# Kernel optimization log

Measured on AMD Instinct MI355X. Metric: run time of the kernel, lower is better.

Reference implementation:

```python
import jax, jax.numpy as jnp
import numpy as np

EPS_XVAR = 1e-06
EPS_QVAR = 1e-05
EPS_VAR = 1e-05
MIN_SCALE = 0.1  # rbf kernel
EPS_EDGE = 1e-06


def setup_inputs() -> dict:
    key = jax.random.key(0)
    k1, k2, k3, k4 = jax.random.split(key, 4)
    B, O, I, M = 2048, 64, 64, 32
    x = jax.random.normal(k1, (B, I), dtype=jnp.float32)
    # inducing locations: linspace(-1.5, 1.5, M) tiled over (O, I)
    z = jnp.broadcast_to(jnp.linspace(-1.5, 1.5, M, dtype=jnp.float32), (O, I, M))
    q_mu = jax.random.normal(k2, (O, I, M), dtype=jnp.float32) * 0.05
    q_log_var = jnp.full((O, I, M), -3.0, dtype=jnp.float32)
    log_scale = jnp.zeros((O, I), dtype=jnp.float32)
    log_variance = jnp.full((O, I), -1.0, dtype=jnp.float32)
    return {"x": x, "z": z, "q_mu": q_mu, "q_log_var": q_log_var,
            "log_scale": log_scale, "log_variance": log_variance}


def reference(x, z, q_mu, q_log_var, log_scale, log_variance):
    # x: [B, I]; params: [O, I, M] or [O, I]
    x_mean = x
    x_var = jnp.zeros_like(x) + EPS_XVAR

    q_var = jnp.maximum(jnp.exp(q_log_var), EPS_QVAR)           # [O, I, M]
    var_kern = jnp.maximum(jnp.exp(log_variance), EPS_VAR)      # [O, I]
    lengthscale = jnp.maximum(jnp.exp(log_scale), MIN_SCALE)    # [O, I]

    x_mu_exp = x_mean[:, None, :, None]        # [B, 1, I, 1]
    x_var_exp = x_var[:, None, :, None]        # [B, 1, I, 1]
    ell_sq = (lengthscale ** 2)[None, :, :, None]  # [1, O, I, 1]
    vk = var_kern[None, :, :, None]            # [1, O, I, 1]

    denom = ell_sq + x_var_exp                 # [B, O, I, 1]
    diff = x_mu_exp - z[None]                  # [B, O, I, M]
    psi_1 = vk * jnp.sqrt(ell_sq / denom) * jnp.exp(-0.5 * diff ** 2 / denom)

    edge_means = jnp.sum(psi_1 * q_mu[None], axis=-1)                      # [B, O, I]
    edge_vars = jnp.sum(psi_1 ** 2 * (q_var + q_mu ** 2)[None], axis=-1)   # [B, O, I]
    edge_vars = jnp.maximum(edge_vars - edge_means ** 2, EPS_EDGE)

    return edge_means.sum(axis=2), edge_vars.sum(axis=2)  # each [B, O]
```

## Files before the change

### kernel.cpp

```cpp
#include <hip/hip_runtime.h>

#define BATCH 2048
#define ODIM 64
#define IDIM 64
#define MDIM 32

static constexpr float LOG2E = 1.4426950408889634f;

#if __has_builtin(__builtin_amdgcn_exp2f)
#define EXP2F(x) __builtin_amdgcn_exp2f(x)
#else
#define EXP2F(x) exp2f(x)
#endif

typedef float v2f __attribute__((ext_vector_type(2)));

__global__ __launch_bounds__(256) void prep_kernel(
    const float* __restrict__ x, const float* __restrict__ z,
    const float* __restrict__ q_mu, const float* __restrict__ q_log_var,
    const float* __restrict__ log_scale, const float* __restrict__ log_variance,
    float2* __restrict__ cm, float4* __restrict__ aux, float* __restrict__ xT)
{
    const int bx = blockIdx.x;
    if (bx < 512) {
        int tid = bx * 256 + threadIdx.x;
        int oi  = tid >> 5;
        int m   = tid & (MDIM - 1);

        float ls   = log_scale[oi];
        float lv   = log_variance[oi];
        float ell  = fmaxf(expf(ls), 0.1f);
        float ell2 = ell * ell;
        float vk   = fmaxf(expf(lv), 1e-5f);
        float denom = ell2 + 1e-6f;
        float A    = vk * sqrtf(ell2 / denom);
        float a    = -0.5f * LOG2E / denom;

        float qm = q_mu[tid];
        float qv = fmaxf(expf(q_log_var[tid]), 1e-5f);

        float zm = z[tid];
        float w  = exp2f(a * zm * zm);

        float2 c;
        c.x = A * qm * w;
        c.y = A * A * (qv + qm * qm) * w * w;
        cm[tid] = c;

        if (m == 0) {
            float z0 = z[oi * MDIM + 0];
            float z1 = z[oi * MDIM + 1];
            float dz = z1 - z0;
            float4 Ax = {a, -2.0f * a * z0, -2.0f * a * dz, 0.0f};
            aux[oi] = Ax;
        }
    } else {
        int tid = (bx - 512) * 256 + threadIdx.x;
        int i = tid >> 11;
        int b = tid & (BATCH - 1);
        xT[tid] = x[b * IDIM + i];
    }
}

__global__ __launch_bounds__(512, 8) void gpkan_main_kernel(
    const float* __restrict__ xT, const float2* __restrict__ cm,
    const float4* __restrict__ aux, float* __restrict__ out)
{
    const int o     = blockIdx.x & (ODIM - 1);
    const int btile = blockIdx.x >> 6;
    const int lane  = threadIdx.x & 63;
    const int wave  = __builtin_amdgcn_readfirstlane(threadIdx.x >> 6);
    const int b0    = btile * 128 + lane;
    const int i0    = wave * 8;

    __shared__ float2 lcm[8][256];
    __shared__ float4 laux[8][8];
    __shared__ float  smr[8][2][64];
    __shared__ float  svr[8][2][64];

    const float2* __restrict__ Cg = cm + ((size_t)o * IDIM + i0) * MDIM;
    #pragma unroll
    for (int r = 0; r < 4; ++r)
        lcm[wave][lane + 64 * r] = Cg[lane + 64 * r];
    if (lane < 8) laux[wave][lane] = aux[o * IDIM + i0 + lane];

    v2f emt = {0.f, 0.f};
    v2f evt = {0.f, 0.f};

    v2f xv;
    xv.x = xT[i0 * BATCH + b0];
    xv.y = xT[i0 * BATCH + b0 + 64];

    #pragma unroll 1
    for (int ii = 0; ii < 8; ++ii) {
        int inext = i0 + ((ii + 1) & 7);
        v2f xn;
        xn.x = xT[inext * BATCH + b0];
        xn.y = xT[inext * BATCH + b0 + 64];

        const float4 Ax = laux[wave][ii];
        v2f e1 = {Ax.x, Ax.x}, e2 = {Ax.y, Ax.y}, rc = {Ax.z, Ax.z};

        v2f t = __builtin_elementwise_fma(e1, xv, e2) * xv;
        v2f Eb;
        Eb.x = EXP2F(t.x); Eb.y = EXP2F(t.y);
        v2f ur = rc * xv;
        v2f rr;
        rr.x = EXP2F(ur.x); rr.y = EXP2F(ur.y);

        v2f s = rr * rr;
        v2f u = s * s;

        v2f Pe = {0.f, 0.f}, Po = {0.f, 0.f};
        v2f Qe = {0.f, 0.f}, Qo = {0.f, 0.f};

        const float4* C = (const float4*)&lcm[wave][ii * MDIM];
        #pragma unroll
        for (int k = 15; k >= 0; --k) {
            float4 c = C[k];
            v2f c1e = {c.x, c.x}, c2e = {c.y, c.y};
            v2f c1o = {c.z, c.z}, c2o = {c.w, c.w};
            Pe = __builtin_elementwise_fma(Pe, s, c1e);
            Po = __builtin_elementwise_fma(Po, s, c1o);
            Qe = __builtin_elementwise_fma(Qe, u, c2e);
            Qo = __builtin_elementwise_fma(Qo, u, c2o);
        }

        v2f P = __builtin_elementwise_fma(rr, Po, Pe);
        v2f Q = __builtin_elementwise_fma(s,  Qo, Qe);

        v2f em_i = Eb * P;
        v2f Eb2  = Eb * Eb;
        v2f ev_i = Eb2 * Q;

        v2f eps = {1e-6f, 1e-6f};
        v2f d   = __builtin_elementwise_fma(-em_i, em_i, ev_i);
        evt += __builtin_elementwise_max(d, eps);
        emt += em_i;

        xv = xn;
    }

    smr[wave][0][lane] = emt.x;
    smr[wave][1][lane] = emt.y;
    svr[wave][0][lane] = evt.x;
    svr[wave][1][lane] = evt.y;
    __syncthreads();

    if (threadIdx.x < 128) {
        const int half = threadIdx.x >> 6;
        const int l    = threadIdx.x & 63;
        float em = 0.f, ev = 0.f;
        #pragma unroll
        for (int w = 0; w < 8; ++w) {
            em += smr[w][half][l];
            ev += svr[w][half][l];
        }
        const int bb = btile * 128 + half * 64 + l;
        out[bb * ODIM + o]                = em;
        out[BATCH * ODIM + bb * ODIM + o] = ev;
    }
}

extern "C" void kernel_launch(void* const* d_in, const int* in_sizes, int n_in,
                              void* d_out, int out_size, void* d_ws, size_t ws_size,
                              hipStream_t stream) {
    const float* x            = (const float*)d_in[0];
    const float* z            = (const float*)d_in[1];
    const float* q_mu         = (const float*)d_in[2];
    const float* q_log_var    = (const float*)d_in[3];
    const float* log_scale    = (const float*)d_in[4];
    const float* log_variance = (const float*)d_in[5];
    float* out = (float*)d_out;

    char* ws = (char*)d_ws;
    float2* cm  = (float2*)ws;
    float4* aux = (float4*)(ws + (size_t)ODIM * IDIM * MDIM * sizeof(float2));
    float*  xT  = (float*)(ws + (size_t)ODIM * IDIM * MDIM * sizeof(float2)
                              + (size_t)ODIM * IDIM * sizeof(float4));

    prep_kernel<<<dim3(1024), dim3(256), 0, stream>>>(
        x, z, q_mu, q_log_var, log_scale, log_variance, cm, aux, xT);
    gpkan_main_kernel<<<dim3((BATCH / 128) * ODIM), dim3(512), 0, stream>>>(
        xT, cm, aux, out);
}
```

Baseline: 83.65 us.

## Fuse parameter prep and x transpose into main kernel via shared memory

Removes the separate prep kernel and its global workspace. Each block now transposes its 128-row x tile into shared memory and computes the per-(o,i,m) coefficients and per-(o,i) aux constants directly into LDS before the main loop. This saves a kernel launch and the global round trip for cm, aux and xT. In exchange every one of the 16 batch tiles recomputes the coefficient exps for its output column, and the larger LDS footprint lowers the launch-bound occupancy target from 8 to 6.

```diff
diff --git a/kernel.cpp b/kernel.cpp
--- a/kernel.cpp
+++ b/kernel.cpp
@@ -15,17 +15,44 @@
 
 typedef float v2f __attribute__((ext_vector_type(2)));
 
-__global__ __launch_bounds__(256) void prep_kernel(
+__global__ __launch_bounds__(512, 6) void gpkan_fused_kernel(
     const float* __restrict__ x, const float* __restrict__ z,
     const float* __restrict__ q_mu, const float* __restrict__ q_log_var,
     const float* __restrict__ log_scale, const float* __restrict__ log_variance,
-    float2* __restrict__ cm, float4* __restrict__ aux, float* __restrict__ xT)
+    float* __restrict__ out)
 {
-    const int bx = blockIdx.x;
-    if (bx < 512) {
-        int tid = bx * 256 + threadIdx.x;
-        int oi  = tid >> 5;
-        int m   = tid & (MDIM - 1);
+    const int o     = blockIdx.x & (ODIM - 1);
+    const int btile = blockIdx.x >> 6;
+    const int tid   = threadIdx.x;
+    const int lane  = tid & 63;
+    const int wave  = __builtin_amdgcn_readfirstlane(tid >> 6);
+
+    __shared__ float  xtile[IDIM][128];
+    __shared__ float2 lcm[IDIM * MDIM];
+    __shared__ float4 laux[IDIM];
+
+    {
+        const int bl = tid >> 2;
+        const int q4 = tid & 3;
+        const float4* xr =
+            (const float4*)(x + (size_t)(btile * 128 + bl) * IDIM + 16 * q4);
+        #pragma unroll
+        for (int j = 0; j < 4; ++j) {
+            float4 v = xr[j];
+            int ib = 16 * q4 + 4 * j;
+            xtile[ib + 0][bl] = v.x;
+            xtile[ib + 1][bl] = v.y;
+            xtile[ib + 2][bl] = v.z;
+            xtile[ib + 3][bl] = v.w;
+        }
+    }
+
+    #pragma unroll
+    for (int k = 0; k < 4; ++k) {
+        int e  = tid + 512 * k;
+        int i  = e >> 5;
+        int oi = o * IDIM + i;
+        int g  = oi * MDIM + (e & (MDIM - 1));
 
         float ls   = log_scale[oi];
         float lv   = log_variance[oi];
@@ -36,69 +63,46 @@
         float A    = vk * sqrtf(ell2 / denom);
         float a    = -0.5f * LOG2E / denom;
 
-        float qm = q_mu[tid];
-        float qv = fmaxf(expf(q_log_var[tid]), 1e-5f);
-
-        float zm = z[tid];
+        float qm = q_mu[g];
+        float qv = fmaxf(expf(q_log_var[g]), 1e-5f);
+        float zm = z[g];
         float w  = exp2f(a * zm * zm);
 
         float2 c;
         c.x = A * qm * w;
         c.y = A * A * (qv + qm * qm) * w * w;
-        cm[tid] = c;
+        lcm[e] = c;
+    }
 
-        if (m == 0) {
-            float z0 = z[oi * MDIM + 0];
-            float z1 = z[oi * MDIM + 1];
-            float dz = z1 - z0;
-            float4 Ax = {a, -2.0f * a * z0, -2.0f * a * dz, 0.0f};
-            aux[oi] = Ax;
-        }
-    } else {
-        int tid = (bx - 512) * 256 + threadIdx.x;
-        int i = tid >> 11;
-        int b = tid & (BATCH - 1);
-        xT[tid] = x[b * IDIM + i];
+    if (tid < IDIM) {
+        int oi = o * IDIM + tid;
+        float ls   = log_scale[oi];
+        float ell  = fmaxf(expf(ls), 0.1f);
+        float denom = ell * ell + 1e-6f;
+        float a    = -0.5f * LOG2E / denom;
+        float z0 = z[oi * MDIM + 0];
+        float z1 = z[oi * MDIM + 1];
+        float dz = z1 - z0;
+        laux[tid] = make_float4(a, -2.0f * a * z0, -2.0f * a * dz, 0.0f);
     }
-}
+    __syncthreads();
 
-__global__ __launch_bounds__(512, 8) void gpkan_main_kernel(
-    const float* __restrict__ xT, const float2* __restrict__ cm,
-    const float4* __restrict__ aux, float* __restrict__ out)
-{
-    const int o     = blockIdx.x & (ODIM - 1);
-    const int btile = blockIdx.x >> 6;
-    const int lane  = threadIdx.x & 63;
-    const int wave  = __builtin_amdgcn_readfirstlane(threadIdx.x >> 6);
-    const int b0    = btile * 128 + lane;
-    const int i0    = wave * 8;
-
-    __shared__ float2 lcm[8][256];
-    __shared__ float4 laux[8][8];
-    __shared__ float  smr[8][2][64];
-    __shared__ float  svr[8][2][64];
-
-    const float2* __restrict__ Cg = cm + ((size_t)o * IDIM + i0) * MDIM;
-    #pragma unroll
-    for (int r = 0; r < 4; ++r)
-        lcm[wave][lane + 64 * r] = Cg[lane + 64 * r];
-    if (lane < 8) laux[wave][lane] = aux[o * IDIM + i0 + lane];
-
+    const int i0 = wave * 8;
     v2f emt = {0.f, 0.f};
     v2f evt = {0.f, 0.f};
 
     v2f xv;
-    xv.x = xT[i0 * BATCH + b0];
-    xv.y = xT[i0 * BATCH + b0 + 64];
+    xv.x = xtile[i0][lane];
+    xv.y = xtile[i0][lane + 64];
 
     #pragma unroll 1
     for (int ii = 0; ii < 8; ++ii) {
         int inext = i0 + ((ii + 1) & 7);
         v2f xn;
-        xn.x = xT[inext * BATCH + b0];
-        xn.y = xT[inext * BATCH + b0 + 64];
+        xn.x = xtile[inext][lane];
+        xn.y = xtile[inext][lane + 64];
 
-        const float4 Ax = laux[wave][ii];
+        const float4 Ax = laux[i0 + ii];
         v2f e1 = {Ax.x, Ax.x}, e2 = {Ax.y, Ax.y}, rc = {Ax.z, Ax.z};
 
         v2f t = __builtin_elementwise_fma(e1, xv, e2) * xv;
@@ -114,7 +118,7 @@
         v2f Pe = {0.f, 0.f}, Po = {0.f, 0.f};
         v2f Qe = {0.f, 0.f}, Qo = {0.f, 0.f};
 
-        const float4* C = (const float4*)&lcm[wave][ii * MDIM];
+        const float4* C = (const float4*)&lcm[(i0 + ii) * MDIM];
         #pragma unroll
         for (int k = 15; k >= 0; --k) {
             float4 c = C[k];
@@ -141,20 +145,23 @@
         xv = xn;
     }
 
-    smr[wave][0][lane] = emt.x;
-    smr[wave][1][lane] = emt.y;
-    svr[wave][0][lane] = evt.x;
-    svr[wave][1][lane] = evt.y;
+    __syncthreads();
+    float* red = &xtile[0][0];
+    float* redv = red + 1024;
+    red [(wave * 2 + 0) * 64 + lane] = emt.x;
+    red [(wave * 2 + 1) * 64 + lane] = emt.y;
+    redv[(wave * 2 + 0) * 64 + lane] = evt.x;
+    redv[(wave * 2 + 1) * 64 + lane] = evt.y;
     __syncthreads();
 
-    if (threadIdx.x < 128) {
-        const int half = threadIdx.x >> 6;
-        const int l    = threadIdx.x & 63;
+    if (tid < 128) {
+        const int half = tid >> 6;
+        const int l    = tid & 63;
         float em = 0.f, ev = 0.f;
         #pragma unroll
         for (int w = 0; w < 8; ++w) {
-            em += smr[w][half][l];
-            ev += svr[w][half][l];
+            em += red [(w * 2 + half) * 64 + l];
+            ev += redv[(w * 2 + half) * 64 + l];
         }
         const int bb = btile * 128 + half * 64 + l;
         out[bb * ODIM + o]                = em;
@@ -173,14 +180,6 @@
     const float* log_variance = (const float*)d_in[5];
     float* out = (float*)d_out;
 
-    char* ws = (char*)d_ws;
-    float2* cm  = (float2*)ws;
-    float4* aux = (float4*)(ws + (size_t)ODIM * IDIM * MDIM * sizeof(float2));
-    float*  xT  = (float*)(ws + (size_t)ODIM * IDIM * MDIM * sizeof(float2)
-                              + (size_t)ODIM * IDIM * sizeof(float4));
-
-    prep_kernel<<<dim3(1024), dim3(256), 0, stream>>>(
-        x, z, q_mu, q_log_var, log_scale, log_variance, cm, aux, xT);
-    gpkan_main_kernel<<<dim3((BATCH / 128) * ODIM), dim3(512), 0, stream>>>(
-        xT, cm, aux, out);
+    gpkan_fused_kernel<<<dim3((BATCH / 128) * ODIM), dim3(512), 0, stream>>>(
+        x, z, q_mu, q_log_var, log_scale, log_variance, out);
 }
```

Measured after the change: 82.53 us. About the same (-1.3%).

## Read coefficients directly from global memory as float4 and preload all x values

Applied to the files above, without the earlier changes.

The main kernel no longer stages per-wave coefficient and aux tables in LDS; each wave reads wave-uniform float4 coefficients straight from global memory, which the compiler can turn into scalar loads. All eight x pairs are preloaded up front as contiguous v2f loads, with lanes now owning adjacent batch elements. The LDS reduction is reorganised into one buffer. The prep kernel writes coefficients two at a time as float4. This removes LDS staging and its traffic, at the cost of more registers and reliance on cache hits for coefficient reads.

```diff
diff --git a/kernel.cpp b/kernel.cpp
--- a/kernel.cpp
+++ b/kernel.cpp
@@ -15,17 +15,19 @@
 
 typedef float v2f __attribute__((ext_vector_type(2)));
 
+
 __global__ __launch_bounds__(256) void prep_kernel(
     const float* __restrict__ x, const float* __restrict__ z,
     const float* __restrict__ q_mu, const float* __restrict__ q_log_var,
     const float* __restrict__ log_scale, const float* __restrict__ log_variance,
-    float2* __restrict__ cm, float4* __restrict__ aux, float* __restrict__ xT)
+    float4* __restrict__ cmq, float4* __restrict__ aux, float* __restrict__ xT)
 {
     const int bx = blockIdx.x;
-    if (bx < 512) {
-        int tid = bx * 256 + threadIdx.x;
-        int oi  = tid >> 5;
-        int m   = tid & (MDIM - 1);
+    if (bx < 256) {
+        int qt = bx * 256 + threadIdx.x;
+        int oi = qt >> 4;
+        int k  = qt & 15;
+        int g  = oi * MDIM + 2 * k;
 
         float ls   = log_scale[oi];
         float lv   = log_variance[oi];
@@ -36,26 +38,28 @@
         float A    = vk * sqrtf(ell2 / denom);
         float a    = -0.5f * LOG2E / denom;
 
-        float qm = q_mu[tid];
-        float qv = fmaxf(expf(q_log_var[tid]), 1e-5f);
+        float qm0 = q_mu[g],     qm1 = q_mu[g + 1];
+        float qv0 = fmaxf(expf(q_log_var[g]),     1e-5f);
+        float qv1 = fmaxf(expf(q_log_var[g + 1]), 1e-5f);
+        float zm0 = z[g],        zm1 = z[g + 1];
+        float w0  = exp2f(a * zm0 * zm0);
+        float w1  = exp2f(a * zm1 * zm1);
 
-        float zm = z[tid];
-        float w  = exp2f(a * zm * zm);
+        float4 c;
+        c.x = A * qm0 * w0;
+        c.y = A * A * (qv0 + qm0 * qm0) * w0 * w0;
+        c.z = A * qm1 * w1;
+        c.w = A * A * (qv1 + qm1 * qm1) * w1 * w1;
+        cmq[qt] = c;
 
-        float2 c;
-        c.x = A * qm * w;
-        c.y = A * A * (qv + qm * qm) * w * w;
-        cm[tid] = c;
-
-        if (m == 0) {
+        if (k == 0) {
             float z0 = z[oi * MDIM + 0];
             float z1 = z[oi * MDIM + 1];
             float dz = z1 - z0;
-            float4 Ax = {a, -2.0f * a * z0, -2.0f * a * dz, 0.0f};
-            aux[oi] = Ax;
+            aux[oi] = make_float4(a, -2.0f * a * z0, -2.0f * a * dz, 0.0f);
         }
     } else {
-        int tid = (bx - 512) * 256 + threadIdx.x;
+        int tid = (bx - 256) * 256 + threadIdx.x;
         int i = tid >> 11;
         int b = tid & (BATCH - 1);
         xT[tid] = x[b * IDIM + i];
@@ -63,48 +67,41 @@
 }
 
 __global__ __launch_bounds__(512, 8) void gpkan_main_kernel(
-    const float* __restrict__ xT, const float2* __restrict__ cm,
+    const float* __restrict__ xT, const float4* __restrict__ cmq,
     const float4* __restrict__ aux, float* __restrict__ out)
 {
     const int o     = blockIdx.x & (ODIM - 1);
     const int btile = blockIdx.x >> 6;
-    const int lane  = threadIdx.x & 63;
-    const int wave  = __builtin_amdgcn_readfirstlane(threadIdx.x >> 6);
-    const int b0    = btile * 128 + lane;
+    const int tid   = threadIdx.x;
+    const int lane  = tid & 63;
+    const int wave  = __builtin_amdgcn_readfirstlane(tid >> 6);
+    const int b0    = btile * 128 + 2 * lane;
     const int i0    = wave * 8;
 
-    __shared__ float2 lcm[8][256];
-    __shared__ float4 laux[8][8];
-    __shared__ float  smr[8][2][64];
-    __shared__ float  svr[8][2][64];
+    __shared__ float red[2][8][128];
 
-    const float2* __restrict__ Cg = cm + ((size_t)o * IDIM + i0) * MDIM;
+    v2f xv[8];
     #pragma unroll
-    for (int r = 0; r < 4; ++r)
-        lcm[wave][lane + 64 * r] = Cg[lane + 64 * r];
-    if (lane < 8) laux[wave][lane] = aux[o * IDIM + i0 + lane];
+    for (int ii = 0; ii < 8; ++ii)
+        xv[ii] = *(const v2f*)&xT[(size_t)(i0 + ii) * BATCH + b0];
+
+    const float4* __restrict__ Cb = cmq + ((size_t)o * IDIM + i0) * 16;
+    const float4* __restrict__ Ab = aux + o * IDIM + i0;
 
     v2f emt = {0.f, 0.f};
     v2f evt = {0.f, 0.f};
 
-    v2f xv;
-    xv.x = xT[i0 * BATCH + b0];
-    xv.y = xT[i0 * BATCH + b0 + 64];
-
     #pragma unroll 1
     for (int ii = 0; ii < 8; ++ii) {
-        int inext = i0 + ((ii + 1) & 7);
-        v2f xn;
-        xn.x = xT[inext * BATCH + b0];
-        xn.y = xT[inext * BATCH + b0 + 64];
+        const float4 Ax = Ab[ii];
+        const v2f x2 = xv[ii];
 
-        const float4 Ax = laux[wave][ii];
         v2f e1 = {Ax.x, Ax.x}, e2 = {Ax.y, Ax.y}, rc = {Ax.z, Ax.z};
 
-        v2f t = __builtin_elementwise_fma(e1, xv, e2) * xv;
+        v2f t = __builtin_elementwise_fma(e1, x2, e2) * x2;
         v2f Eb;
         Eb.x = EXP2F(t.x); Eb.y = EXP2F(t.y);
-        v2f ur = rc * xv;
+        v2f ur = rc * x2;
         v2f rr;
         rr.x = EXP2F(ur.x); rr.y = EXP2F(ur.y);
 
@@ -114,7 +111,7 @@
         v2f Pe = {0.f, 0.f}, Po = {0.f, 0.f};
         v2f Qe = {0.f, 0.f}, Qo = {0.f, 0.f};
 
-        const float4* C = (const float4*)&lcm[wave][ii * MDIM];
+        const float4* C = Cb + ii * 16;
         #pragma unroll
         for (int k = 15; k >= 0; --k) {
             float4 c = C[k];
@@ -130,35 +127,29 @@
         v2f Q = __builtin_elementwise_fma(s,  Qo, Qe);
 
         v2f em_i = Eb * P;
-        v2f Eb2  = Eb * Eb;
-        v2f ev_i = Eb2 * Q;
+        v2f ev_i = (Eb * Eb) * Q;
 
         v2f eps = {1e-6f, 1e-6f};
         v2f d   = __builtin_elementwise_fma(-em_i, em_i, ev_i);
         evt += __builtin_elementwise_max(d, eps);
         emt += em_i;
-
-        xv = xn;
     }
 
-    smr[wave][0][lane] = emt.x;
-    smr[wave][1][lane] = emt.y;
-    svr[wave][0][lane] = evt.x;
-    svr[wave][1][lane] = evt.y;
+    red[0][wave][2 * lane + 0] = emt.x;
+    red[0][wave][2 * lane + 1] = emt.y;
+    red[1][wave][2 * lane + 0] = evt.x;
+    red[1][wave][2 * lane + 1] = evt.y;
     __syncthreads();
 
-    if (threadIdx.x < 128) {
-        const int half = threadIdx.x >> 6;
-        const int l    = threadIdx.x & 63;
-        float em = 0.f, ev = 0.f;
+    if (tid < 256) {
+        const int sel = tid >> 7;
+        const int l   = tid & 127;
+        float acc = 0.f;
         #pragma unroll
-        for (int w = 0; w < 8; ++w) {
-            em += smr[w][half][l];
-            ev += svr[w][half][l];
-        }
-        const int bb = btile * 128 + half * 64 + l;
-        out[bb * ODIM + o]                = em;
-        out[BATCH * ODIM + bb * ODIM + o] = ev;
+        for (int w = 0; w < 8; ++w) acc += red[sel][w][l];
+        const int bb = btile * 128 + l;
+        if (sel == 0) out[bb * ODIM + o] = acc;
+        else          out[BATCH * ODIM + bb * ODIM + o] = acc;
     }
 }
 
@@ -174,13 +165,13 @@
     float* out = (float*)d_out;
 
     char* ws = (char*)d_ws;
-    float2* cm  = (float2*)ws;
-    float4* aux = (float4*)(ws + (size_t)ODIM * IDIM * MDIM * sizeof(float2));
-    float*  xT  = (float*)(ws + (size_t)ODIM * IDIM * MDIM * sizeof(float2)
+    float4* cmq = (float4*)ws;
+    float4* aux = (float4*)(ws + (size_t)ODIM * IDIM * 16 * sizeof(float4));
+    float*  xT  = (float*)(ws + (size_t)ODIM * IDIM * 16 * sizeof(float4)
                               + (size_t)ODIM * IDIM * sizeof(float4));
 
-    prep_kernel<<<dim3(1024), dim3(256), 0, stream>>>(
-        x, z, q_mu, q_log_var, log_scale, log_variance, cm, aux, xT);
+    prep_kernel<<<dim3(768), dim3(256), 0, stream>>>(
+        x, z, q_mu, q_log_var, log_scale, log_variance, cmq, aux, xT);
     gpkan_main_kernel<<<dim3((BATCH / 128) * ODIM), dim3(512), 0, stream>>>(
-        xT, cm, aux, out);
+        xT, cmq, aux, out);
 }
```

New measurement: 81.79 us. 1.02x faster.
